# Kernel tuning notes

Measured on AMD Instinct MI355X. Metric: run time of the kernel, lower is better.

The kernel has to match this reference:

```python
import jax, jax.numpy as jnp
import numpy as np

N_HEADS = 12
B, S, D = 2, 2048, 768
NEG = -1e9


def setup_inputs() -> dict:
    key = jax.random.key(0)
    ks = jax.random.split(key, 7)
    scale = 1.0 / np.sqrt(D)
    Q = jax.random.normal(ks[0], (B, S, D), jnp.float32)
    K = jax.random.normal(ks[1], (B, S, D), jnp.float32)
    V = jax.random.normal(ks[2], (B, S, D), jnp.float32)
    # causal mask, broadcastable over batch and heads; 0 entries are masked out
    mask = jnp.tril(jnp.ones((S, S), jnp.int32))[None, None, :, :]
    Wq = jax.random.normal(ks[3], (D, D), jnp.float32) * scale
    Wk = jax.random.normal(ks[4], (D, D), jnp.float32) * scale
    Wv = jax.random.normal(ks[5], (D, D), jnp.float32) * scale
    Wo = jax.random.normal(ks[6], (D, D), jnp.float32) * scale
    return {"Q": Q, "K": K, "V": V, "mask": mask,
            "Wq": Wq, "Wk": Wk, "Wv": Wv, "Wo": Wo}


def reference(Q, K, V, mask, Wq, Wk, Wv, Wo):
    b, s, d = Q.shape
    h = N_HEADS
    dk = d // h
    # projections (torch nn.Linear: x @ W.T), split heads -> (b, h, s, dk)
    q = (Q @ Wq.T).reshape(b, s, h, dk).transpose(0, 2, 1, 3)
    k = (K @ Wk.T).reshape(b, s, h, dk).transpose(0, 2, 1, 3)
    v = (V @ Wv.T).reshape(b, s, h, dk).transpose(0, 2, 1, 3)
    scores = jnp.einsum('bhqd,bhkd->bhqk', q, k) / jnp.sqrt(jnp.asarray(dk, q.dtype))
    scores = jnp.where(mask == 0, jnp.asarray(NEG, scores.dtype), scores)
    attn = jax.nn.softmax(scores, axis=-1)  # dropout p=0.0 -> identity
    ctx = jnp.einsum('bhqk,bhkd->bhqd', attn, v)
    ctx = ctx.transpose(0, 2, 1, 3).reshape(b, s, d)
    return ctx @ Wo.T
```

## Files before the change

kernel.cpp:

```cpp
#include <hip/hip_runtime.h>
#include <math.h>

#define NH     12
#define BB     2
#define SEQ    2048
#define DMODEL 768
#define DK     64

typedef __attribute__((ext_vector_type(8))) short short8;
typedef __attribute__((ext_vector_type(4))) float floatx4;

__device__ __forceinline__ unsigned short f2bf(float x) {
    unsigned u = __builtin_bit_cast(unsigned, x);
    u = (u + 0x7fffu + ((u >> 16) & 1u)) >> 16;
    return (unsigned short)u;
}
__device__ __forceinline__ unsigned short f2bf_fast(float x) {
    unsigned u = __builtin_bit_cast(unsigned, x);
    return (unsigned short)((u + 0x8000u) >> 16);
}
__device__ __forceinline__ float bf2f(unsigned short h) {
    unsigned u = ((unsigned)h) << 16;
    return __builtin_bit_cast(float, u);
}

__device__ __forceinline__ void gld_lds16(const ushort* gptr, ushort* lptr) {
    __builtin_amdgcn_global_load_lds(
        (const __attribute__((address_space(1))) unsigned int*)(const void*)gptr,
        (__attribute__((address_space(3))) unsigned int*)(void*)lptr,
        16, 0, 0);
}

#define SI (BB * SEQ * DMODEL)
#define SW (DMODEL * DMODEL)

__global__ __launch_bounds__(256) void cast_all(
    const float* __restrict__ Q, const float* __restrict__ K, const float* __restrict__ V,
    const float* __restrict__ Wq, const float* __restrict__ Wk, const float* __restrict__ Wv,
    const float* __restrict__ Wo,
    ushort* oQ, ushort* oK, ushort* oV, ushort* oWq, ushort* oWk, ushort* oWv, ushort* oWo) {
    long i = (long)(blockIdx.x * 256 + threadIdx.x) * 4;
    const float* src; ushort* dst; long off;
    if      (i < 1L * SI)          { src = Q;  dst = oQ;  off = i; }
    else if (i < 2L * SI)          { src = K;  dst = oK;  off = i - 1L * SI; }
    else if (i < 3L * SI)          { src = V;  dst = oV;  off = i - 2L * SI; }
    else if (i < 3L * SI + SW)     { src = Wq; dst = oWq; off = i - 3L * SI; }
    else if (i < 3L * SI + 2L*SW)  { src = Wk; dst = oWk; off = i - 3L * SI - SW; }
    else if (i < 3L * SI + 3L*SW)  { src = Wv; dst = oWv; off = i - 3L * SI - 2L * SW; }
    else                           { src = Wo; dst = oWo; off = i - 3L * SI - 3L * SW; }
    float4 v = *(const float4*)(src + off);
    ushort4 o;
    o.x = f2bf(v.x); o.y = f2bf(v.y); o.z = f2bf(v.z); o.w = f2bf(v.w);
    *(ushort4*)(dst + off) = o;
}

template<int MODE>
__device__ __forceinline__ void gemm_body(const ushort* __restrict__ A,
                                          const ushort* __restrict__ W,
                                          float* __restrict__ outF,
                                          ushort* __restrict__ outH,
                                          float scale) {
    const int n0 = blockIdx.x * 128;
    const int m0 = blockIdx.y * 128;
    const int tid  = threadIdx.x;
    const int lane = tid & 63;
    const int wv   = tid >> 6;
    const int l15  = lane & 15;
    const int quad = lane >> 4;
    const int wm = (wv >> 1) * 64;
    const int wn = (wv & 1) * 64;

    __shared__ ushort S[2][2][128 * 64];

    const int srow = tid >> 3;
    const int scol = (tid & 7) * 8;

    floatx4 acc[4][4];
    #pragma unroll
    for (int i = 0; i < 4; ++i)
        #pragma unroll
        for (int j = 0; j < 4; ++j) acc[i][j] = (floatx4)0.f;

    #pragma unroll
    for (int it = 0; it < 4; ++it) {
        const int r = srow + it * 32;
        gld_lds16(A + (size_t)(m0 + r) * DMODEL + scol, &S[0][0][r * 64 + scol]);
        gld_lds16(W + (size_t)(n0 + r) * DMODEL + scol, &S[0][1][r * 64 + scol]);
    }

    for (int t = 0; t < DMODEL / 64; ++t) {
        __syncthreads();
        if (t + 1 < DMODEL / 64) {
            const int k0 = (t + 1) * 64;
            const int bi = (t + 1) & 1;
            #pragma unroll
            for (int it = 0; it < 4; ++it) {
                const int r = srow + it * 32;
                gld_lds16(A + (size_t)(m0 + r) * DMODEL + k0 + scol, &S[bi][0][r * 64 + scol]);
                gld_lds16(W + (size_t)(n0 + r) * DMODEL + k0 + scol, &S[bi][1][r * 64 + scol]);
            }
        }
        const ushort* As  = S[t & 1][0];
        const ushort* Ws2 = S[t & 1][1];
        #pragma unroll
        for (int kc = 0; kc < 2; ++kc) {
            short8 af[4], bf[4];
            #pragma unroll
            for (int mi = 0; mi < 4; ++mi)
                af[mi] = *(const short8*)&As[(wm + mi * 16 + l15) * 64 + kc * 32 + quad * 8];
            #pragma unroll
            for (int ni = 0; ni < 4; ++ni)
                bf[ni] = *(const short8*)&Ws2[(wn + ni * 16 + l15) * 64 + kc * 32 + quad * 8];
            #pragma unroll
            for (int mi = 0; mi < 4; ++mi)
                #pragma unroll
                for (int ni = 0; ni < 4; ++ni)
                    acc[mi][ni] = __builtin_amdgcn_mfma_f32_16x16x32_bf16(af[mi], bf[ni], acc[mi][ni], 0, 0, 0);
        }
    }

    #pragma unroll
    for (int mi = 0; mi < 4; ++mi)
        #pragma unroll
        for (int ni = 0; ni < 4; ++ni)
            #pragma unroll
            for (int r = 0; r < 4; ++r) {
                const int m = m0 + wm + mi * 16 + quad * 4 + r;
                const int n = n0 + wn + ni * 16 + l15;
                const float v = acc[mi][ni][r] * scale;
                if (MODE == 0) {
                    outF[(size_t)m * DMODEL + n] = v;
                } else {
                    const int b = m >> 11, s = m & (SEQ - 1);
                    const int h = n >> 6,  dk = n & 63;
                    outH[(((size_t)b * NH + h) * SEQ + s) * DK + dk] = f2bf(v);
                }
            }
}

#define QSCALE (0.125f * 1.44269504088896f)

__global__ __launch_bounds__(256) void gemm_qkv(
    const ushort* Qb, const ushort* Kb, const ushort* Vb,
    const ushort* Wqb, const ushort* Wkb, const ushort* Wvb,
    ushort* qh, ushort* kh, ushort* vh) {
    const int z = blockIdx.z;
    const ushort* A = (z == 0) ? Qb : (z == 1) ? Kb : Vb;
    const ushort* W = (z == 0) ? Wqb : (z == 1) ? Wkb : Wvb;
    ushort* out     = (z == 0) ? qh : (z == 1) ? kh : vh;
    const float scale = (z == 0) ? QSCALE : 1.0f;
    gemm_body<1>(A, W, nullptr, out, scale);
}

__global__ __launch_bounds__(256) void gemm_out(const ushort* A, const ushort* W, float* out) {
    gemm_body<0>(A, W, out, nullptr, 1.0f);
}

__global__ __launch_bounds__(256) void transpose_v(const ushort* __restrict__ vh,
                                                   ushort* __restrict__ vhT) {
    const int bh = blockIdx.y;
    const int s0 = blockIdx.x * 64;
    __shared__ float T[64][65];
    const int t = threadIdx.x;
    {
        const int row = t >> 2, c16 = (t & 3) * 16;
        const ushort* src = vh + ((size_t)bh * SEQ + s0 + row) * DK + c16;
        short8 v0 = *(const short8*)(src);
        short8 v1 = *(const short8*)(src + 8);
        #pragma unroll
        for (int i = 0; i < 8; ++i) {
            T[row][c16 + i]     = bf2f((unsigned short)v0[i]);
            T[row][c16 + 8 + i] = bf2f((unsigned short)v1[i]);
        }
    }
    __syncthreads();
    {
        const int dk = t >> 2, sc = (t & 3) * 16;
        short8 o0, o1;
        #pragma unroll
        for (int i = 0; i < 8; ++i) {
            o0[i] = (short)f2bf(T[sc + i][dk]);
            o1[i] = (short)f2bf(T[sc + 8 + i][dk]);
        }
        ushort* dst = vhT + ((size_t)bh * DK + dk) * SEQ + s0 + sc;
        *(short8*)(dst)     = o0;
        *(short8*)(dst + 8) = o1;
    }
}

__global__ __launch_bounds__(256) void flash_mfma(const ushort* __restrict__ qh,
                                                  const ushort* __restrict__ kh,
                                                  const ushort* __restrict__ vhT,
                                                  ushort* __restrict__ ctx) {
    const int bh = blockIdx.x;
    const int b  = bh / NH, h = bh % NH;
    const int qt = (gridDim.y - 1) - blockIdx.y;
    const int q0 = qt * 64;

    const int tid  = threadIdx.x;
    const int lane = tid & 63;
    const int wv   = tid >> 6;
    const int l15  = lane & 15;
    const int quad = lane >> 4;

    __shared__ ushort KV[2][2][64 * 64];
    __shared__ ushort Ps[4][16 * 72];

    const ushort* kbase = kh  + (size_t)bh * SEQ * DK;
    const ushort* vbase = vhT + (size_t)bh * DK * SEQ;

    const int srow = tid >> 3;
    const int scol = (tid & 7) * 8;

    short8 q_frag[2];
    {
        const ushort* qp = qh + ((size_t)bh * SEQ + q0 + wv * 16 + l15) * DK;
        q_frag[0] = *(const short8*)(qp + quad * 8);
        q_frag[1] = *(const short8*)(qp + 32 + quad * 8);
    }

    {
        gld_lds16(kbase + (size_t)(srow) * DK + scol,            &KV[0][0][srow * 64 + scol]);
        gld_lds16(kbase + (size_t)(srow + 32) * DK + scol,       &KV[0][0][(srow + 32) * 64 + scol]);
        gld_lds16(vbase + (size_t)srow * SEQ + scol,             &KV[0][1][srow * 64 + scol]);
        gld_lds16(vbase + (size_t)(srow + 32) * SEQ + scol,      &KV[0][1][(srow + 32) * 64 + scol]);
    }

    float m_r[4], l_r[4];
    floatx4 o_acc[4];
    #pragma unroll
    for (int r = 0; r < 4; ++r) { m_r[r] = -3.0e38f; l_r[r] = 0.f; }
    #pragma unroll
    for (int d = 0; d < 4; ++d) o_acc[d] = (floatx4)0.f;

    for (int kt = 0; kt <= qt; ++kt) {
        __syncthreads();
        if (kt < qt) {
            const int k0 = (kt + 1) * 64;
            const int bi = (kt + 1) & 1;
            gld_lds16(kbase + (size_t)(k0 + srow) * DK + scol,        &KV[bi][0][srow * 64 + scol]);
            gld_lds16(kbase + (size_t)(k0 + srow + 32) * DK + scol,   &KV[bi][0][(srow + 32) * 64 + scol]);
            gld_lds16(vbase + (size_t)srow * SEQ + k0 + scol,         &KV[bi][1][srow * 64 + scol]);
            gld_lds16(vbase + (size_t)(srow + 32) * SEQ + k0 + scol,  &KV[bi][1][(srow + 32) * 64 + scol]);
        }
        const ushort* Ks  = KV[kt & 1][0];
        const ushort* Vts = KV[kt & 1][1];

        floatx4 s_acc[4];
        #pragma unroll
        for (int nt = 0; nt < 4; ++nt) s_acc[nt] = (floatx4)0.f;
        #pragma unroll
        for (int kc = 0; kc < 2; ++kc)
            #pragma unroll
            for (int nt = 0; nt < 4; ++nt) {
                short8 kf = *(const short8*)&Ks[(nt * 16 + l15) * 64 + kc * 32 + quad * 8];
                s_acc[nt] = __builtin_amdgcn_mfma_f32_16x16x32_bf16(q_frag[kc], kf, s_acc[nt], 0, 0, 0);
            }

        if (kt == qt) {
            #pragma unroll
            for (int nt = 0; nt < 4; ++nt)
                #pragma unroll
                for (int r = 0; r < 4; ++r) {
                    const int col  = nt * 16 + l15;
                    const int rowl = wv * 16 + quad * 4 + r;
                    if (col > rowl) s_acc[nt][r] = -1.0e30f;
                }
        }

        float alpha[4];
        #pragma unroll
        for (int r = 0; r < 4; ++r) {
            float mx = fmaxf(fmaxf(s_acc[0][r], s_acc[1][r]), fmaxf(s_acc[2][r], s_acc[3][r]));
            #pragma unroll
            for (int d = 1; d < 16; d <<= 1) mx = fmaxf(mx, __shfl_xor(mx, d));
            const float mnew = fmaxf(m_r[r], mx);
            alpha[r] = exp2f(m_r[r] - mnew);
            m_r[r] = mnew;
            float rs = 0.f;
            #pragma unroll
            for (int nt = 0; nt < 4; ++nt) {
                const float p = exp2f(s_acc[nt][r] - mnew);
                s_acc[nt][r] = p;
                rs += p;
            }
            #pragma unroll
            for (int d = 1; d < 16; d <<= 1) rs += __shfl_xor(rs, d);
            l_r[r] = l_r[r] * alpha[r] + rs;
        }
        #pragma unroll
        for (int d = 0; d < 4; ++d)
            #pragma unroll
            for (int r = 0; r < 4; ++r) o_acc[d][r] *= alpha[r];

        #pragma unroll
        for (int nt = 0; nt < 4; ++nt)
            #pragma unroll
            for (int r = 0; r < 4; ++r)
                Ps[wv][(quad * 4 + r) * 72 + nt * 16 + l15] = f2bf_fast(s_acc[nt][r]);

        #pragma unroll
        for (int kc = 0; kc < 2; ++kc) {
            short8 pf = *(const short8*)&Ps[wv][l15 * 72 + kc * 32 + quad * 8];
            #pragma unroll
            for (int dkt = 0; dkt < 4; ++dkt) {
                short8 vf = *(const short8*)&Vts[(dkt * 16 + l15) * 64 + kc * 32 + quad * 8];
                o_acc[dkt] = __builtin_amdgcn_mfma_f32_16x16x32_bf16(pf, vf, o_acc[dkt], 0, 0, 0);
            }
        }
    }

    #pragma unroll
    for (int r = 0; r < 4; ++r) {
        const float inv = 1.f / l_r[r];
        const int s = q0 + wv * 16 + quad * 4 + r;
        #pragma unroll
        for (int dkt = 0; dkt < 4; ++dkt) {
            const int d = h * DK + dkt * 16 + l15;
            ctx[((size_t)b * SEQ + s) * DMODEL + d] = f2bf(o_acc[dkt][r] * inv);
        }
    }
}

extern "C" void kernel_launch(void* const* d_in, const int* in_sizes, int n_in,
                              void* d_out, int out_size, void* d_ws, size_t ws_size,
                              hipStream_t stream) {
    const float* Q  = (const float*)d_in[0];
    const float* K  = (const float*)d_in[1];
    const float* V  = (const float*)d_in[2];
    const float* Wq = (const float*)d_in[4];
    const float* Wk = (const float*)d_in[5];
    const float* Wv = (const float*)d_in[6];
    const float* Wo = (const float*)d_in[7];

    char* ws = (char*)d_ws;
    const size_t SZ_IN = (size_t)SI * 2;
    const size_t SZ_W  = (size_t)SW * 2;
    ushort* Qbf = (ushort*)(ws);
    ushort* Kbf = (ushort*)(ws + SZ_IN);
    ushort* Vbf = (ushort*)(ws + 2 * SZ_IN);
    ushort* Wqb = (ushort*)(ws + 3 * SZ_IN);
    ushort* Wkb = (ushort*)(ws + 3 * SZ_IN + SZ_W);
    ushort* Wvb = (ushort*)(ws + 3 * SZ_IN + 2 * SZ_W);
    ushort* Wob = (ushort*)(ws + 3 * SZ_IN + 3 * SZ_W);
    ushort* qh  = (ushort*)(ws + 3 * SZ_IN + 4 * SZ_W);
    ushort* kh  = (ushort*)(ws + 4 * SZ_IN + 4 * SZ_W);
    ushort* vh  = (ushort*)(ws + 5 * SZ_IN + 4 * SZ_W);
    ushort* vhT = Kbf;
    ushort* ctx = Qbf;

    dim3 blk(256);
    cast_all<<<dim3((3 * SI + 4 * SW) / 1024), blk, 0, stream>>>(
        Q, K, V, Wq, Wk, Wv, Wo, Qbf, Kbf, Vbf, Wqb, Wkb, Wvb, Wob);
    gemm_qkv<<<dim3(6, 32, 3), blk, 0, stream>>>(Qbf, Kbf, Vbf, Wqb, Wkb, Wvb, qh, kh, vh);
    transpose_v<<<dim3(32, 24), blk, 0, stream>>>(vh, vhT);
    flash_mfma<<<dim3(24, 32), blk, 0, stream>>>(qh, kh, vhT, ctx);
    gemm_out<<<dim3(6, 32), blk, 0, stream>>>(ctx, Wob, (float*)d_out);
}
```

Before: 232.2 us.

## Fuse V transpose into QKV GEMM, swizzle LDS, add atomic work queue to flash

The V projection now writes its output directly in transposed layout through an operand-swapped MFMA path, which removes the separate transpose kernel and its extra round trip through memory. The GEMM shrinks its K-tile to 32 and XOR-swizzles the LDS chunks, and the flash kernel also swizzles its K/V tiles to cut bank conflicts. The flash kernel computes S transposed so each lane holds a whole query row, which reduces the row-reduction shuffles. It also pulls work items from an atomic counter, largest causal tiles first. This adds a memset and atomic traffic, and the smaller GEMM K-tile doubles the number of barriers.

```diff
diff --git a/kernel.cpp b/kernel.cpp
--- a/kernel.cpp
+++ b/kernel.cpp
@@ -8,6 +8,7 @@
 #define DK     64
 
 typedef __attribute__((ext_vector_type(8))) short short8;
+typedef __attribute__((ext_vector_type(4))) short short4v;
 typedef __attribute__((ext_vector_type(4))) float floatx4;
 
 __device__ __forceinline__ unsigned short f2bf(float x) {
@@ -18,10 +19,6 @@
 __device__ __forceinline__ unsigned short f2bf_fast(float x) {
     unsigned u = __builtin_bit_cast(unsigned, x);
     return (unsigned short)((u + 0x8000u) >> 16);
-}
-__device__ __forceinline__ float bf2f(unsigned short h) {
-    unsigned u = ((unsigned)h) << 16;
-    return __builtin_bit_cast(float, u);
 }
 
 __device__ __forceinline__ void gld_lds16(const ushort* gptr, ushort* lptr) {
@@ -70,10 +67,12 @@
     const int wm = (wv >> 1) * 64;
     const int wn = (wv & 1) * 64;
 
-    __shared__ ushort S[2][2][128 * 64];
-
-    const int srow = tid >> 3;
-    const int scol = (tid & 7) * 8;
+    __shared__ __align__(16) ushort S[2][2][128 * 32];
+
+    const int srow = tid >> 2;
+    const int sch  = tid & 3;
+    const int schx = sch ^ ((srow >> 1) & 3);
+    const int sw2  = (l15 >> 1) & 3;
 
     floatx4 acc[4][4];
     #pragma unroll
@@ -82,41 +81,42 @@
         for (int j = 0; j < 4; ++j) acc[i][j] = (floatx4)0.f;
 
     #pragma unroll
-    for (int it = 0; it < 4; ++it) {
-        const int r = srow + it * 32;
-        gld_lds16(A + (size_t)(m0 + r) * DMODEL + scol, &S[0][0][r * 64 + scol]);
-        gld_lds16(W + (size_t)(n0 + r) * DMODEL + scol, &S[0][1][r * 64 + scol]);
+    for (int it = 0; it < 2; ++it) {
+        const int r = srow + it * 64;
+        gld_lds16(A + (size_t)(m0 + r) * DMODEL + schx * 8, &S[0][0][r * 32 + sch * 8]);
+        gld_lds16(W + (size_t)(n0 + r) * DMODEL + schx * 8, &S[0][1][r * 32 + sch * 8]);
     }
 
-    for (int t = 0; t < DMODEL / 64; ++t) {
+    for (int t = 0; t < DMODEL / 32; ++t) {
         __syncthreads();
-        if (t + 1 < DMODEL / 64) {
-            const int k0 = (t + 1) * 64;
+        if (t + 1 < DMODEL / 32) {
+            const int k0 = (t + 1) * 32;
             const int bi = (t + 1) & 1;
             #pragma unroll
-            for (int it = 0; it < 4; ++it) {
-                const int r = srow + it * 32;
-                gld_lds16(A + (size_t)(m0 + r) * DMODEL + k0 + scol, &S[bi][0][r * 64 + scol]);
-                gld_lds16(W + (size_t)(n0 + r) * DMODEL + k0 + scol, &S[bi][1][r * 64 + scol]);
+            for (int it = 0; it < 2; ++it) {
+                const int r = srow + it * 64;
+                gld_lds16(A + (size_t)(m0 + r) * DMODEL + k0 + schx * 8, &S[bi][0][r * 32 + sch * 8]);
+                gld_lds16(W + (size_t)(n0 + r) * DMODEL + k0 + schx * 8, &S[bi][1][r * 32 + sch * 8]);
             }
         }
         const ushort* As  = S[t & 1][0];
         const ushort* Ws2 = S[t & 1][1];
-        #pragma unroll
-        for (int kc = 0; kc < 2; ++kc) {
-            short8 af[4], bf[4];
-            #pragma unroll
-            for (int mi = 0; mi < 4; ++mi)
-                af[mi] = *(const short8*)&As[(wm + mi * 16 + l15) * 64 + kc * 32 + quad * 8];
-            #pragma unroll
-            for (int ni = 0; ni < 4; ++ni)
-                bf[ni] = *(const short8*)&Ws2[(wn + ni * 16 + l15) * 64 + kc * 32 + quad * 8];
-            #pragma unroll
-            for (int mi = 0; mi < 4; ++mi)
-                #pragma unroll
-                for (int ni = 0; ni < 4; ++ni)
+        short8 af[4], bf[4];
+        #pragma unroll
+        for (int mi = 0; mi < 4; ++mi)
+            af[mi] = *(const short8*)&As[(wm + mi * 16 + l15) * 32 + ((quad ^ sw2) * 8)];
+        #pragma unroll
+        for (int ni = 0; ni < 4; ++ni)
+            bf[ni] = *(const short8*)&Ws2[(wn + ni * 16 + l15) * 32 + ((quad ^ sw2) * 8)];
+        #pragma unroll
+        for (int mi = 0; mi < 4; ++mi)
+            #pragma unroll
+            for (int ni = 0; ni < 4; ++ni) {
+                if (MODE == 2)
+                    acc[mi][ni] = __builtin_amdgcn_mfma_f32_16x16x32_bf16(bf[ni], af[mi], acc[mi][ni], 0, 0, 0);
+                else
                     acc[mi][ni] = __builtin_amdgcn_mfma_f32_16x16x32_bf16(af[mi], bf[ni], acc[mi][ni], 0, 0, 0);
-        }
+            }
     }
 
     #pragma unroll
@@ -125,15 +125,23 @@
         for (int ni = 0; ni < 4; ++ni)
             #pragma unroll
             for (int r = 0; r < 4; ++r) {
-                const int m = m0 + wm + mi * 16 + quad * 4 + r;
-                const int n = n0 + wn + ni * 16 + l15;
                 const float v = acc[mi][ni][r] * scale;
-                if (MODE == 0) {
-                    outF[(size_t)m * DMODEL + n] = v;
-                } else {
+                if (MODE == 2) {
+                    const int m = m0 + wm + mi * 16 + l15;
+                    const int n = n0 + wn + ni * 16 + quad * 4 + r;
                     const int b = m >> 11, s = m & (SEQ - 1);
                     const int h = n >> 6,  dk = n & 63;
-                    outH[(((size_t)b * NH + h) * SEQ + s) * DK + dk] = f2bf(v);
+                    outH[(((size_t)b * NH + h) * DK + dk) * SEQ + s] = f2bf(v);
+                } else {
+                    const int m = m0 + wm + mi * 16 + quad * 4 + r;
+                    const int n = n0 + wn + ni * 16 + l15;
+                    if (MODE == 0) {
+                        outF[(size_t)m * DMODEL + n] = v;
+                    } else {
+                        const int b = m >> 11, s = m & (SEQ - 1);
+                        const int h = n >> 6,  dk = n & 63;
+                        outH[(((size_t)b * NH + h) * SEQ + s) * DK + dk] = f2bf(v);
+                    }
                 }
             }
 }
@@ -143,181 +151,156 @@
 __global__ __launch_bounds__(256) void gemm_qkv(
     const ushort* Qb, const ushort* Kb, const ushort* Vb,
     const ushort* Wqb, const ushort* Wkb, const ushort* Wvb,
-    ushort* qh, ushort* kh, ushort* vh) {
+    ushort* qh, ushort* kh, ushort* vhT) {
     const int z = blockIdx.z;
-    const ushort* A = (z == 0) ? Qb : (z == 1) ? Kb : Vb;
-    const ushort* W = (z == 0) ? Wqb : (z == 1) ? Wkb : Wvb;
-    ushort* out     = (z == 0) ? qh : (z == 1) ? kh : vh;
-    const float scale = (z == 0) ? QSCALE : 1.0f;
-    gemm_body<1>(A, W, nullptr, out, scale);
+    if (z == 0)      gemm_body<1>(Qb, Wqb, nullptr, qh,  QSCALE);
+    else if (z == 1) gemm_body<1>(Kb, Wkb, nullptr, kh,  1.0f);
+    else             gemm_body<2>(Vb, Wvb, nullptr, vhT, 1.0f);
 }
 
 __global__ __launch_bounds__(256) void gemm_out(const ushort* A, const ushort* W, float* out) {
     gemm_body<0>(A, W, out, nullptr, 1.0f);
 }
 
-__global__ __launch_bounds__(256) void transpose_v(const ushort* __restrict__ vh,
-                                                   ushort* __restrict__ vhT) {
-    const int bh = blockIdx.y;
-    const int s0 = blockIdx.x * 64;
-    __shared__ float T[64][65];
-    const int t = threadIdx.x;
-    {
-        const int row = t >> 2, c16 = (t & 3) * 16;
-        const ushort* src = vh + ((size_t)bh * SEQ + s0 + row) * DK + c16;
-        short8 v0 = *(const short8*)(src);
-        short8 v1 = *(const short8*)(src + 8);
-        #pragma unroll
-        for (int i = 0; i < 8; ++i) {
-            T[row][c16 + i]     = bf2f((unsigned short)v0[i]);
-            T[row][c16 + 8 + i] = bf2f((unsigned short)v1[i]);
-        }
-    }
-    __syncthreads();
-    {
-        const int dk = t >> 2, sc = (t & 3) * 16;
-        short8 o0, o1;
-        #pragma unroll
-        for (int i = 0; i < 8; ++i) {
-            o0[i] = (short)f2bf(T[sc + i][dk]);
-            o1[i] = (short)f2bf(T[sc + 8 + i][dk]);
-        }
-        ushort* dst = vhT + ((size_t)bh * DK + dk) * SEQ + s0 + sc;
-        *(short8*)(dst)     = o0;
-        *(short8*)(dst + 8) = o1;
-    }
-}
+#define NITEMS (24 * 32)
 
 __global__ __launch_bounds__(256) void flash_mfma(const ushort* __restrict__ qh,
                                                   const ushort* __restrict__ kh,
                                                   const ushort* __restrict__ vhT,
-                                                  ushort* __restrict__ ctx) {
-    const int bh = blockIdx.x;
-    const int b  = bh / NH, h = bh % NH;
-    const int qt = (gridDim.y - 1) - blockIdx.y;
-    const int q0 = qt * 64;
-
+                                                  ushort* __restrict__ ctx,
+                                                  int* __restrict__ counter) {
     const int tid  = threadIdx.x;
     const int lane = tid & 63;
     const int wv   = tid >> 6;
     const int l15  = lane & 15;
     const int quad = lane >> 4;
 
-    __shared__ ushort KV[2][2][64 * 64];
-    __shared__ ushort Ps[4][16 * 72];
-
-    const ushort* kbase = kh  + (size_t)bh * SEQ * DK;
-    const ushort* vbase = vhT + (size_t)bh * DK * SEQ;
+    __shared__ __align__(16) ushort KV[2][2][64 * 64];
+    __shared__ __align__(16) ushort Ps[4][16 * 72];
+    __shared__ int wshare;
 
     const int srow = tid >> 3;
-    const int scol = (tid & 7) * 8;
-
-    short8 q_frag[2];
-    {
-        const ushort* qp = qh + ((size_t)bh * SEQ + q0 + wv * 16 + l15) * DK;
-        q_frag[0] = *(const short8*)(qp + quad * 8);
-        q_frag[1] = *(const short8*)(qp + 32 + quad * 8);
-    }
-
-    {
-        gld_lds16(kbase + (size_t)(srow) * DK + scol,            &KV[0][0][srow * 64 + scol]);
-        gld_lds16(kbase + (size_t)(srow + 32) * DK + scol,       &KV[0][0][(srow + 32) * 64 + scol]);
-        gld_lds16(vbase + (size_t)srow * SEQ + scol,             &KV[0][1][srow * 64 + scol]);
-        gld_lds16(vbase + (size_t)(srow + 32) * SEQ + scol,      &KV[0][1][(srow + 32) * 64 + scol]);
-    }
-
-    float m_r[4], l_r[4];
-    floatx4 o_acc[4];
-    #pragma unroll
-    for (int r = 0; r < 4; ++r) { m_r[r] = -3.0e38f; l_r[r] = 0.f; }
-    #pragma unroll
-    for (int d = 0; d < 4; ++d) o_acc[d] = (floatx4)0.f;
-
-    for (int kt = 0; kt <= qt; ++kt) {
+    const int sch  = tid & 7;
+    const int schx = sch ^ (srow & 7);
+    const int swq  = l15 & 7;
+
+    for (;;) {
+        if (tid == 0) wshare = atomicAdd(counter, 1);
         __syncthreads();
-        if (kt < qt) {
-            const int k0 = (kt + 1) * 64;
-            const int bi = (kt + 1) & 1;
-            gld_lds16(kbase + (size_t)(k0 + srow) * DK + scol,        &KV[bi][0][srow * 64 + scol]);
-            gld_lds16(kbase + (size_t)(k0 + srow + 32) * DK + scol,   &KV[bi][0][(srow + 32) * 64 + scol]);
-            gld_lds16(vbase + (size_t)srow * SEQ + k0 + scol,         &KV[bi][1][srow * 64 + scol]);
-            gld_lds16(vbase + (size_t)(srow + 32) * SEQ + k0 + scol,  &KV[bi][1][(srow + 32) * 64 + scol]);
+        const int w = wshare;
+        if (w >= NITEMS) break;
+        const int qt = 31 - (w / 24);
+        const int bh = w - (w / 24) * 24;
+        const int b  = bh / NH, h = bh % NH;
+        const int q0 = qt * 64;
+
+        const ushort* kbase = kh  + (size_t)bh * SEQ * DK;
+        const ushort* vbase = vhT + (size_t)bh * DK * SEQ;
+
+        short8 q_frag[2];
+        {
+            const ushort* qp = qh + ((size_t)bh * SEQ + q0 + wv * 16 + l15) * DK;
+            q_frag[0] = *(const short8*)(qp + quad * 8);
+            q_frag[1] = *(const short8*)(qp + 32 + quad * 8);
         }
-        const ushort* Ks  = KV[kt & 1][0];
-        const ushort* Vts = KV[kt & 1][1];
-
-        floatx4 s_acc[4];
-        #pragma unroll
-        for (int nt = 0; nt < 4; ++nt) s_acc[nt] = (floatx4)0.f;
-        #pragma unroll
-        for (int kc = 0; kc < 2; ++kc)
+
+        gld_lds16(kbase + (size_t)srow * DK + schx * 8,        &KV[0][0][srow * 64 + sch * 8]);
+        gld_lds16(kbase + (size_t)(srow + 32) * DK + schx * 8, &KV[0][0][(srow + 32) * 64 + sch * 8]);
+        gld_lds16(vbase + (size_t)srow * SEQ + schx * 8,       &KV[0][1][srow * 64 + sch * 8]);
+        gld_lds16(vbase + (size_t)(srow + 32) * SEQ + schx * 8,&KV[0][1][(srow + 32) * 64 + sch * 8]);
+
+        float m_s = -3.0e38f, l_s = 0.f;
+        floatx4 o_acc[4];
+        #pragma unroll
+        for (int d = 0; d < 4; ++d) o_acc[d] = (floatx4)0.f;
+
+        for (int kt = 0; kt <= qt; ++kt) {
+            __syncthreads();
+            if (kt < qt) {
+                const int k0 = (kt + 1) * 64;
+                const int bi = (kt + 1) & 1;
+                gld_lds16(kbase + (size_t)(k0 + srow) * DK + schx * 8,        &KV[bi][0][srow * 64 + sch * 8]);
+                gld_lds16(kbase + (size_t)(k0 + srow + 32) * DK + schx * 8,   &KV[bi][0][(srow + 32) * 64 + sch * 8]);
+                gld_lds16(vbase + (size_t)srow * SEQ + k0 + schx * 8,         &KV[bi][1][srow * 64 + sch * 8]);
+                gld_lds16(vbase + (size_t)(srow + 32) * SEQ + k0 + schx * 8,  &KV[bi][1][(srow + 32) * 64 + sch * 8]);
+            }
+            const ushort* Ks  = KV[kt & 1][0];
+            const ushort* Vts = KV[kt & 1][1];
+
+            floatx4 s_acc[4];
+            #pragma unroll
+            for (int nt = 0; nt < 4; ++nt) s_acc[nt] = (floatx4)0.f;
+            #pragma unroll
+            for (int kc = 0; kc < 2; ++kc)
+                #pragma unroll
+                for (int nt = 0; nt < 4; ++nt) {
+                    short8 kf = *(const short8*)&Ks[(nt * 16 + l15) * 64 + (((kc * 4 + quad) ^ swq) * 8)];
+                    s_acc[nt] = __builtin_amdgcn_mfma_f32_16x16x32_bf16(kf, q_frag[kc], s_acc[nt], 0, 0, 0);
+                }
+
+            if (kt == qt) {
+                const int ql = wv * 16 + l15;
+                #pragma unroll
+                for (int nt = 0; nt < 4; ++nt)
+                    #pragma unroll
+                    for (int r = 0; r < 4; ++r)
+                        if (nt * 16 + quad * 4 + r > ql) s_acc[nt][r] = -1.0e30f;
+            }
+
+            float mx = s_acc[0][0];
+            #pragma unroll
+            for (int nt = 0; nt < 4; ++nt)
+                #pragma unroll
+                for (int r = 0; r < 4; ++r) mx = fmaxf(mx, s_acc[nt][r]);
+            mx = fmaxf(mx, __shfl_xor(mx, 16));
+            mx = fmaxf(mx, __shfl_xor(mx, 32));
+            const float mnew = fmaxf(m_s, mx);
+            const float al = exp2f(m_s - mnew);
+            m_s = mnew;
+            float rs = 0.f;
             #pragma unroll
             for (int nt = 0; nt < 4; ++nt) {
-                short8 kf = *(const short8*)&Ks[(nt * 16 + l15) * 64 + kc * 32 + quad * 8];
-                s_acc[nt] = __builtin_amdgcn_mfma_f32_16x16x32_bf16(q_frag[kc], kf, s_acc[nt], 0, 0, 0);
-            }
-
-        if (kt == qt) {
-            #pragma unroll
-            for (int nt = 0; nt < 4; ++nt)
+                short4v pk;
                 #pragma unroll
                 for (int r = 0; r < 4; ++r) {
-                    const int col  = nt * 16 + l15;
-                    const int rowl = wv * 16 + quad * 4 + r;
-                    if (col > rowl) s_acc[nt][r] = -1.0e30f;
+                    const float p = exp2f(s_acc[nt][r] - mnew);
+                    rs += p;
+                    pk[r] = (short)f2bf_fast(p);
                 }
+                *(short4v*)&Ps[wv][l15 * 72 + nt * 16 + quad * 4] = pk;
+            }
+            rs += __shfl_xor(rs, 16);
+            rs += __shfl_xor(rs, 32);
+            l_s = l_s * al + rs;
+
+            #pragma unroll
+            for (int r = 0; r < 4; ++r) {
+                const float ar = __shfl(al, quad * 20 + r);
+                #pragma unroll
+                for (int d = 0; d < 4; ++d) o_acc[d][r] *= ar;
+            }
+
+            #pragma unroll
+            for (int kc = 0; kc < 2; ++kc) {
+                short8 pf = *(const short8*)&Ps[wv][l15 * 72 + kc * 32 + quad * 8];
+                #pragma unroll
+                for (int dkt = 0; dkt < 4; ++dkt) {
+                    short8 vf = *(const short8*)&Vts[(dkt * 16 + l15) * 64 + (((kc * 4 + quad) ^ swq) * 8)];
+                    o_acc[dkt] = __builtin_amdgcn_mfma_f32_16x16x32_bf16(pf, vf, o_acc[dkt], 0, 0, 0);
+                }
+            }
         }
 
-        float alpha[4];
         #pragma unroll
         for (int r = 0; r < 4; ++r) {
-            float mx = fmaxf(fmaxf(s_acc[0][r], s_acc[1][r]), fmaxf(s_acc[2][r], s_acc[3][r]));
-            #pragma unroll
-            for (int d = 1; d < 16; d <<= 1) mx = fmaxf(mx, __shfl_xor(mx, d));
-            const float mnew = fmaxf(m_r[r], mx);
-            alpha[r] = exp2f(m_r[r] - mnew);
-            m_r[r] = mnew;
-            float rs = 0.f;
-            #pragma unroll
-            for (int nt = 0; nt < 4; ++nt) {
-                const float p = exp2f(s_acc[nt][r] - mnew);
-                s_acc[nt][r] = p;
-                rs += p;
-            }
-            #pragma unroll
-            for (int d = 1; d < 16; d <<= 1) rs += __shfl_xor(rs, d);
-            l_r[r] = l_r[r] * alpha[r] + rs;
-        }
-        #pragma unroll
-        for (int d = 0; d < 4; ++d)
-            #pragma unroll
-            for (int r = 0; r < 4; ++r) o_acc[d][r] *= alpha[r];
-
-        #pragma unroll
-        for (int nt = 0; nt < 4; ++nt)
-            #pragma unroll
-            for (int r = 0; r < 4; ++r)
-                Ps[wv][(quad * 4 + r) * 72 + nt * 16 + l15] = f2bf_fast(s_acc[nt][r]);
-
-        #pragma unroll
-        for (int kc = 0; kc < 2; ++kc) {
-            short8 pf = *(const short8*)&Ps[wv][l15 * 72 + kc * 32 + quad * 8];
+            const float lr = __shfl(l_s, quad * 20 + r);
+            const float inv = 1.f / lr;
+            const int s = q0 + wv * 16 + quad * 4 + r;
             #pragma unroll
             for (int dkt = 0; dkt < 4; ++dkt) {
-                short8 vf = *(const short8*)&Vts[(dkt * 16 + l15) * 64 + kc * 32 + quad * 8];
-                o_acc[dkt] = __builtin_amdgcn_mfma_f32_16x16x32_bf16(pf, vf, o_acc[dkt], 0, 0, 0);
-            }
-        }
-    }
-
-    #pragma unroll
-    for (int r = 0; r < 4; ++r) {
-        const float inv = 1.f / l_r[r];
-        const int s = q0 + wv * 16 + quad * 4 + r;
-        #pragma unroll
-        for (int dkt = 0; dkt < 4; ++dkt) {
-            const int d = h * DK + dkt * 16 + l15;
-            ctx[((size_t)b * SEQ + s) * DMODEL + d] = f2bf(o_acc[dkt][r] * inv);
+                const int d = h * DK + dkt * 16 + l15;
+                ctx[((size_t)b * SEQ + s) * DMODEL + d] = f2bf(o_acc[dkt][r] * inv);
+            }
         }
     }
 }
@@ -345,15 +328,15 @@
     ushort* Wob = (ushort*)(ws + 3 * SZ_IN + 3 * SZ_W);
     ushort* qh  = (ushort*)(ws + 3 * SZ_IN + 4 * SZ_W);
     ushort* kh  = (ushort*)(ws + 4 * SZ_IN + 4 * SZ_W);
-    ushort* vh  = (ushort*)(ws + 5 * SZ_IN + 4 * SZ_W);
-    ushort* vhT = Kbf;
+    ushort* vhT = (ushort*)(ws + 5 * SZ_IN + 4 * SZ_W);
+    int*    ctr = (int*)   (ws + 6 * SZ_IN + 4 * SZ_W);
     ushort* ctx = Qbf;
 
     dim3 blk(256);
     cast_all<<<dim3((3 * SI + 4 * SW) / 1024), blk, 0, stream>>>(
         Q, K, V, Wq, Wk, Wv, Wo, Qbf, Kbf, Vbf, Wqb, Wkb, Wvb, Wob);
-    gemm_qkv<<<dim3(6, 32, 3), blk, 0, stream>>>(Qbf, Kbf, Vbf, Wqb, Wkb, Wvb, qh, kh, vh);
-    transpose_v<<<dim3(32, 24), blk, 0, stream>>>(vh, vhT);
-    flash_mfma<<<dim3(24, 32), blk, 0, stream>>>(qh, kh, vhT, ctx);
+    hipMemsetAsync(ctr, 0, sizeof(int), stream);
+    gemm_qkv<<<dim3(6, 32, 3), blk, 0, stream>>>(Qbf, Kbf, Vbf, Wqb, Wkb, Wvb, qh, kh, vhT);
+    flash_mfma<<<dim3(768), blk, 0, stream>>>(qh, kh, vhT, ctx, ctr);
     gemm_out<<<dim3(6, 32), blk, 0, stream>>>(ctx, Wob, (float*)d_out);
 }
```

Result: no change. 227.9 us (-1.9%).
